# Optimization experiments

Hardware: AMD Instinct MI355X
Metric: run time of the kernel (lower is better)

The kernel has to match this reference:

```python
import jax, jax.numpy as jnp
import numpy as np

D_MODEL = 1024
HEAD_DIM = 64
NUM_HEADS = 16
NUM_KV_HEADS = 4
LOGIT_CAP = 50.0
F_EMBED = 10000


def rope(inputs, positions, head_dim, max_wavelength):
    # inputs: [B, T, N, H]; positions: [B, T]
    fraction = 2.0 * jnp.arange(head_dim // 2, dtype=jnp.float32) / head_dim
    timescale = max_wavelength ** fraction  # [H/2]
    sinusoid = positions.astype(jnp.float32)[..., None] / timescale  # [B, T, H/2]
    sinusoid = sinusoid[..., None, :]  # [B, T, 1, H/2]
    sin, cos = jnp.sin(sinusoid), jnp.cos(sinusoid)
    first, second = jnp.split(inputs, 2, axis=-1)
    return jnp.concatenate([first * cos - second * sin,
                            second * cos + first * sin], axis=-1)


def setup_inputs() -> dict:
    key = jax.random.key(0)
    kx, kq, kkv, ko = jax.random.split(key, 4)
    B, T = 1, 2048
    x = jax.random.normal(kx, (B, T, D_MODEL), dtype=jnp.float32)
    pos = jnp.broadcast_to(jnp.arange(T, dtype=jnp.int32)[None, :], (B, T))
    # mask semantics: True == masked out (logit set to -100). Causal: disallow s > t.
    mask = jnp.broadcast_to(jnp.triu(jnp.ones((T, T), dtype=bool), k=1)[None], (B, T, T))
    sq = 1.0 / np.sqrt(D_MODEL)
    wq = jax.random.normal(kq, (NUM_HEADS, D_MODEL, HEAD_DIM), dtype=jnp.float32) * sq
    wkv = jax.random.normal(kkv, (2, NUM_KV_HEADS, D_MODEL, HEAD_DIM), dtype=jnp.float32) * sq
    wout = jax.random.normal(ko, (NUM_HEADS, HEAD_DIM, D_MODEL), dtype=jnp.float32) * sq
    return {"x": x, "pos": pos, "mask": mask, "wq": wq, "wkv": wkv, "wout": wout}


def reference(x, pos, mask, wq, wkv, wout):
    B, T, _ = x.shape
    K, G = NUM_KV_HEADS, NUM_HEADS // NUM_KV_HEADS
    # projections
    q = jnp.einsum('BTD,NDH->BTNH', x, wq)  # [B,T,N,H]
    q = rope(q, pos, HEAD_DIM, F_EMBED) / jnp.sqrt(jnp.float32(HEAD_DIM))
    kv = jnp.einsum('BSD,CKDH->CBSKH', x, wkv)  # [2,B,S,K,H]
    k_proj, v_proj = kv[0], kv[1]
    k_proj = rope(k_proj, pos, HEAD_DIM, F_EMBED)
    # grouped logits
    qg = q.reshape(B, T, K, G, HEAD_DIM)
    logits = jnp.einsum('BTKGH,BSKH->BTKGS', qg, k_proj).reshape(B, T, NUM_HEADS, T)
    # soft-cap + mask (True in mask => masked => -100)
    logits = jnp.tanh(logits / LOGIT_CAP) * LOGIT_CAP
    logits = jnp.where(~mask[:, :, None, :], logits, -100.0)
    probs = jax.nn.softmax(logits, axis=-1).astype(k_proj.dtype)
    # grouped outer
    pg = probs.reshape(B, T, K, G, T)
    enc = jnp.einsum('BTKGS,BSKH->BTKGH', pg, v_proj).reshape(B, T, NUM_HEADS, HEAD_DIM)
    return jnp.einsum('BTNH,NHD->BTD', enc, wout)
```

## Files before the change

### kernel.cpp

```cpp
#include <hip/hip_runtime.h>
#include <hip/hip_bf16.h>
#include <cstdint>

#define T_SEQ 2048
#define DM    1024
#define HD    64
#define NH    16
#define NKV   4

typedef __attribute__((ext_vector_type(8))) short short8;
typedef __attribute__((ext_vector_type(4))) short short4v;
typedef __attribute__((ext_vector_type(2))) short short2v;
typedef __attribute__((ext_vector_type(4))) float f32x4;

__device__ __forceinline__ unsigned short f2bf(float f) {
    union { float f; unsigned u; } v; v.f = f;
    unsigned r = v.u + 0x7FFF + ((v.u >> 16) & 1);
    return (unsigned short)(r >> 16);
}

__device__ __forceinline__ void gload16(const unsigned short* gp, unsigned short* lp) {
    __builtin_amdgcn_global_load_lds(
        (const __attribute__((address_space(1))) unsigned int*)gp,
        (__attribute__((address_space(3))) unsigned int*)lp, 16, 0, 0);
}

__global__ __launch_bounds__(256) void prep_kernel(const float* __restrict__ x,
                                                   const int* __restrict__ pos,
                                                   const float* __restrict__ wq,
                                                   const float* __restrict__ wkv,
                                                   const float* __restrict__ wout,
                                                   unsigned short* __restrict__ xb,
                                                   float2* __restrict__ stab,
                                                   unsigned short* __restrict__ wqkvT,
                                                   unsigned short* __restrict__ woutT) {
    __shared__ unsigned short tile[64][65];
    int bid = blockIdx.x;
    if (bid < 1024) {
        int i = bid * 256 + threadIdx.x;
        const f32x4* xv = (const f32x4*)x + i * 2;
        f32x4 v0 = xv[0], v1 = xv[1];
        short8 o;
        #pragma unroll
        for (int j = 0; j < 4; j++) { o[j] = (short)f2bf(v0[j]); o[4 + j] = (short)f2bf(v1[j]); }
        *(short8*)(xb + i * 8) = o;
        if (i < 65536) {
            int tt = i >> 5, hm = i & 31;
            float ang = (float)pos[tt] * exp2f((float)hm * -0.41524101186092029f);
            float sv, cv;
            sincosf(ang, &sv, &cv);
            stab[i] = make_float2(sv, cv);
        }
    } else {
        int bid2 = bid - 1024;
        int d0 = (bid2 & 15) * 64;
        int bz = bid2 >> 4;
        int tc = threadIdx.x & 63, tr = threadIdx.x >> 6;
        int tc2 = threadIdx.x & 31, tr2 = threadIdx.x >> 5;
        if (bz < 24) {
            const float* src = (bz < 16) ? (wq + bz * 65536) : (wkv + (bz - 16) * 65536);
            #pragma unroll
            for (int rr = 0; rr < 64; rr += 4)
                tile[rr + tr][tc] = f2bf(src[(d0 + rr + tr) * 64 + tc]);
            __syncthreads();
            #pragma unroll
            for (int rr = 0; rr < 64; rr += 8) {
                int row = rr + tr2;
                short2v o2 = { (short)tile[2 * tc2][row], (short)tile[2 * tc2 + 1][row] };
                *(short2v*)&wqkvT[(bz * 64 + row) * 1024 + d0 + 2 * tc2] = o2;
            }
        } else {
            int j0 = (bz - 24) * 64;
            #pragma unroll
            for (int rr = 0; rr < 64; rr += 4)
                tile[rr + tr][tc] = f2bf(wout[(j0 + rr + tr) * 1024 + d0 + tc]);
            __syncthreads();
            #pragma unroll
            for (int rr = 0; rr < 64; rr += 8) {
                int row = rr + tr2;
                short2v o2 = { (short)tile[2 * tc2][row], (short)tile[2 * tc2 + 1][row] };
                *(short2v*)&woutT[(d0 + row) * 1024 + j0 + 2 * tc2] = o2;
            }
        }
    }
}

__global__ __launch_bounds__(256) void gemm_qkv(const unsigned short* __restrict__ A,
                                                const unsigned short* __restrict__ Bt,
                                                const float2* __restrict__ stab,
                                                unsigned short* __restrict__ qb,
                                                unsigned short* __restrict__ kb2,
                                                unsigned short* __restrict__ vT) {
    __shared__ unsigned short lA[2][4096];
    __shared__ unsigned short lB[2][4096];
    __shared__ float etile[64][65];

    int wid = threadIdx.x >> 6;
    int lane = threadIdx.x & 63;
    int l15 = lane & 15, g = lane >> 4;
    int wr = wid >> 1, wc = wid & 1;
    int r0 = blockIdx.x * 64;
    int by = blockIdx.y;
    int c0 = by * 64;

    f32x4 acc[2][2];
    #pragma unroll
    for (int m = 0; m < 2; m++)
        #pragma unroll
        for (int n = 0; n < 2; n++)
            acc[m][n] = (f32x4){0.f, 0.f, 0.f, 0.f};

    auto stage = [&](int buf, int k0) {
        #pragma unroll
        for (int chunk = 0; chunk < 2; chunk++) {
            int off = threadIdx.x * 16;
            int row = off >> 6, koff = (off & 63) >> 1;
            gload16(A + (r0 + row) * DM + k0 + chunk * 32 + koff,
                    &lA[buf][chunk * 2048 + (off >> 1)]);
            gload16(Bt + (c0 + row) * DM + k0 + chunk * 32 + koff,
                    &lB[buf][chunk * 2048 + (off >> 1)]);
        }
    };

    stage(0, 0);
    __syncthreads();
    for (int k0 = 0; k0 < DM; k0 += 64) {
        int buf = (k0 >> 6) & 1;
        if (k0 + 64 < DM) stage(buf ^ 1, k0 + 64);
        #pragma unroll
        for (int chunk = 0; chunk < 2; chunk++) {
            short8 af[2], bfr[2];
            #pragma unroll
            for (int m = 0; m < 2; m++)
                af[m] = *(const short8*)&lA[buf][chunk * 2048 + (wr * 32 + m * 16 + l15) * 32 + g * 8];
            #pragma unroll
            for (int n = 0; n < 2; n++)
                bfr[n] = *(const short8*)&lB[buf][chunk * 2048 + (wc * 32 + n * 16 + l15) * 32 + g * 8];
            __builtin_amdgcn_s_setprio(1);
            #pragma unroll
            for (int m = 0; m < 2; m++)
                #pragma unroll
                for (int n = 0; n < 2; n++)
                    acc[m][n] = __builtin_amdgcn_mfma_f32_16x16x32_bf16(af[m], bfr[n], acc[m][n], 0, 0, 0);
            __builtin_amdgcn_s_setprio(0);
        }
        __syncthreads();
    }

    #pragma unroll
    for (int m = 0; m < 2; m++)
        #pragma unroll
        for (int n = 0; n < 2; n++)
            #pragma unroll
            for (int rr = 0; rr < 4; rr++)
                etile[wr * 32 + m * 16 + g * 4 + rr][wc * 32 + n * 16 + l15] = acc[m][n][rr];
    __syncthreads();

    if (by < 20) {
        int row = threadIdx.x >> 2;
        int h0 = (threadIdx.x & 3) * 16;
        int t = r0 + row;
        float res[16];
        #pragma unroll
        for (int j = 0; j < 16; j++) {
            int h = h0 + j;
            float val = etile[row][h];
            float oth = etile[row][h ^ 32];
            float2 sc = stab[t * 32 + (h & 31)];
            res[j] = (h < 32) ? (val * sc.y - oth * sc.x) : (val * sc.y + oth * sc.x);
        }
        if (by < 16) {
            short8 o[2];
            #pragma unroll
            for (int j = 0; j < 16; j++) o[j >> 3][j & 7] = (short)f2bf(res[j] * 0.125f);
            unsigned short* qrow = qb + t * 1024 + by * 64 + h0;
            *(short8*)qrow = o[0];
            *(short8*)(qrow + 8) = o[1];
        } else {
            int kvh = by - 16;
            int swz = (t & 7) << 3;
            short8 o[2];
            #pragma unroll
            for (int j = 0; j < 16; j++) o[j >> 3][j & 7] = (short)f2bf(res[j]);
            unsigned short* krow = kb2 + kvh * (T_SEQ * 64) + t * 64;
            *(short8*)(krow + (h0 ^ swz)) = o[0];
            *(short8*)(krow + ((h0 + 8) ^ swz)) = o[1];
        }
    } else {
        int cgl = threadIdx.x >> 2;
        int u0 = (threadIdx.x & 3) * 16;
        int cglob = (by - 20) * 64 + cgl;
        int cx = cgl & 7;
        short8 o[2];
        #pragma unroll
        for (int j = 0; j < 16; j++) {
            int u = u0 + j;
            int chunk = u >> 3, qin = u & 7;
            int hi = qin >> 2, r = qin & 3;
            int sg = chunk ^ cx;
            int tl = (sg >> 2) * 32 + hi * 16 + (sg & 3) * 4 + r;
            o[j >> 3][j & 7] = (short)f2bf(etile[tl][cgl]);
        }
        unsigned short* vrow = vT + cglob * 2048 + r0 + u0;
        *(short8*)vrow = o[0];
        *(short8*)(vrow + 8) = o[1];
    }
}

template<int BM, int BN, int BK>
__global__ __launch_bounds__(256) void gemm_lds(const unsigned short* __restrict__ A,
                                                const unsigned short* __restrict__ Bt,
                                                float* __restrict__ C,
                                                int K, int lda, int ldb, int ldc) {
    constexpr int MR = BM / 32;
    constexpr int NC = BN / 32;
    constexpr int NCH = BK / 32;
    __shared__ unsigned short lA[2][BM * BK];
    __shared__ unsigned short lB[2][BN * BK];

    int wid = threadIdx.x >> 6;
    int lane = threadIdx.x & 63;
    int l15 = lane & 15, g = lane >> 4;
    int wr = wid >> 1, wc = wid & 1;
    int r0 = blockIdx.x * BM;
    int c0 = blockIdx.y * BN;

    f32x4 acc[MR][NC];
    #pragma unroll
    for (int m = 0; m < MR; m++)
        #pragma unroll
        for (int n = 0; n < NC; n++)
            acc[m][n] = (f32x4){0.f, 0.f, 0.f, 0.f};

    auto stage = [&](int buf, int k0) {
        #pragma unroll
        for (int chunk = 0; chunk < NCH; chunk++) {
            #pragma unroll
            for (int i = 0; i < BM / 64; i++) {
                int off = i * 4096 + threadIdx.x * 16;
                int row = off >> 6, koff = (off & 63) >> 1;
                gload16(A + (r0 + row) * lda + k0 + chunk * 32 + koff,
                        &lA[buf][chunk * BM * 32 + (off >> 1)]);
            }
            #pragma unroll
            for (int i = 0; i < BN / 64; i++) {
                int off = i * 4096 + threadIdx.x * 16;
                int row = off >> 6, koff = (off & 63) >> 1;
                gload16(Bt + (c0 + row) * ldb + k0 + chunk * 32 + koff,
                        &lB[buf][chunk * BN * 32 + (off >> 1)]);
            }
        }
    };

    stage(0, 0);
    __syncthreads();
    for (int k0 = 0; k0 < K; k0 += BK) {
        int buf = (k0 / BK) & 1;
        if (k0 + BK < K) stage(buf ^ 1, k0 + BK);
        #pragma unroll
        for (int chunk = 0; chunk < NCH; chunk++) {
            short8 af[MR], bfr[NC];
            #pragma unroll
            for (int m = 0; m < MR; m++)
                af[m] = *(const short8*)&lA[buf][chunk * BM * 32 + (wr * (BM / 2) + m * 16 + l15) * 32 + g * 8];
            #pragma unroll
            for (int n = 0; n < NC; n++)
                bfr[n] = *(const short8*)&lB[buf][chunk * BN * 32 + (wc * (BN / 2) + n * 16 + l15) * 32 + g * 8];
            __builtin_amdgcn_s_setprio(1);
            #pragma unroll
            for (int m = 0; m < MR; m++)
                #pragma unroll
                for (int n = 0; n < NC; n++)
                    acc[m][n] = __builtin_amdgcn_mfma_f32_16x16x32_bf16(af[m], bfr[n], acc[m][n], 0, 0, 0);
            __builtin_amdgcn_s_setprio(0);
        }
        __syncthreads();
    }
    #pragma unroll
    for (int m = 0; m < MR; m++) {
        int row = r0 + wr * (BM / 2) + m * 16 + g * 4;
        #pragma unroll
        for (int n = 0; n < NC; n++) {
            int col = c0 + wc * (BN / 2) + n * 16 + l15;
            #pragma unroll
            for (int rr = 0; rr < 4; rr++)
                C[(row + rr) * ldc + col] = acc[m][n][rr];
        }
    }
}

__global__ __launch_bounds__(512, 4) void attn_kernel(const unsigned short* __restrict__ qb,
                                                      const unsigned short* __restrict__ kb2,
                                                      const unsigned short* __restrict__ vT,
                                                      unsigned short* __restrict__ enc) {
    __shared__ unsigned short lk[2][8192];
    __shared__ unsigned short lv[2][8192];
    __shared__ float s_lc[3][4][16];

    int u = blockIdx.x;
    int kvh = u & 3;
    int j = u >> 2;
    int qt = (j < 64) ? j : (191 - j);
    int wid = threadIdx.x >> 6;
    int lane = threadIdx.x & 63;
    int l15 = lane & 15, g = lane >> 4;
    int hp = wid >> 2;
    int c = wid & 3;
    int q0 = qt * 16;
    int t = q0 + l15;
    int head0 = kvh * 4 + hp * 2;

    short8 qf0[2], qf1[2];
    #pragma unroll
    for (int e = 0; e < 2; e++) {
        const unsigned short* qrow = qb + t * 1024 + (head0 + e) * 64;
        qf0[e] = *(const short8*)(qrow + g * 8);
        qf1[e] = *(const short8*)(qrow + 32 + g * 8);
    }

    f32x4 acc[2][4];
    #pragma unroll
    for (int e = 0; e < 2; e++)
        #pragma unroll
        for (int ht = 0; ht < 4; ht++)
            acc[e][ht] = (f32x4){0.f, 0.f, 0.f, 0.f};
    float lrun[2] = {0.f, 0.f};
    int nph = qt / 8 + 1;

    auto stage = [&](int buf, int s0) {
        #pragma unroll
        for (int i = 0; i < 4; i++) {
            if (wid < 4) {
                int seg = wid * 4 + i;
                gload16(kb2 + kvh * (T_SEQ * 64) + s0 * 64 + seg * 512 + lane * 8,
                        &lk[buf][seg * 512]);
            } else {
                int sv = (wid - 4) * 4 + i;
                int h = sv * 4 + (lane >> 4);
                gload16(vT + (kvh * 64 + h) * T_SEQ + s0 + (lane & 15) * 8,
                        &lv[buf][sv * 512]);
            }
        }
    };

    stage(0, 0);
    __syncthreads();

    for (int ph = 0; ph < nph; ph++) {
        int buf = ph & 1;
        if (ph + 1 < nph) stage(buf ^ 1, (ph + 1) * 128);
        int s0c = ph * 128 + c * 32;
        if (s0c <= q0 + 15) {
            bool needmask = (s0c + 31 > q0);
            union PU { short8 s8; unsigned w[4]; } pf[2];
            #pragma unroll
            for (int uu = 0; uu < 2; uu++) {
                int srow = c * 32 + uu * 16 + l15;
                int swz = (srow & 7) << 3;
                short8 kf0 = *(const short8*)(&lk[buf][srow * 64 + ((g * 8) ^ swz)]);
                short8 kf1 = *(const short8*)(&lk[buf][srow * 64 + ((32 + g * 8) ^ swz)]);
                #pragma unroll
                for (int e = 0; e < 2; e++) {
                    f32x4 z = {0.f, 0.f, 0.f, 0.f};
                    __builtin_amdgcn_s_setprio(1);
                    z = __builtin_amdgcn_mfma_f32_16x16x32_bf16(kf0, qf0[e], z, 0, 0, 0);
                    z = __builtin_amdgcn_mfma_f32_16x16x32_bf16(kf1, qf1[e], z, 0, 0, 0);
                    __builtin_amdgcn_s_setprio(0);
                    float pv[4];
                    #pragma unroll
                    for (int r = 0; r < 4; r++) {
                        float x = z[r];
                        float xc = fmaf(x * x, x * (-1.3333333e-4f), x);
                        float pe = __builtin_amdgcn_exp2f(xc * 1.44269504f);
                        if (needmask) {
                            int s = s0c + uu * 16 + 4 * g + r;
                            pe = (s <= t) ? pe : 0.f;
                        }
                        lrun[e] += pe;
                        pv[r] = pe;
                    }
                    unsigned pk0, pk1;
                    asm("v_cvt_pk_bf16_f32 %0, %1, %2" : "=v"(pk0) : "v"(pv[0]), "v"(pv[1]));
                    asm("v_cvt_pk_bf16_f32 %0, %1, %2" : "=v"(pk1) : "v"(pv[2]), "v"(pv[3]));
                    pf[e].w[uu * 2] = pk0;
                    pf[e].w[uu * 2 + 1] = pk1;
                }
            }
            __builtin_amdgcn_s_setprio(1);
            #pragma unroll
            for (int ht = 0; ht < 4; ht++) {
                int h = ht * 16 + l15;
                short8 vf = *(const short8*)(&lv[buf][h * 128 + (c >> 1) * 64 +
                                                      (((c & 1) * 32 + g * 8) ^ ((h & 7) << 3))]);
                #pragma unroll
                for (int e = 0; e < 2; e++)
                    acc[e][ht] = __builtin_amdgcn_mfma_f32_16x16x32_bf16(vf, pf[e].s8, acc[e][ht], 0, 0, 0);
            }
            __builtin_amdgcn_s_setprio(0);
        }
        __syncthreads();
    }

    #pragma unroll
    for (int e = 0; e < 2; e++) {
        lrun[e] += __shfl_xor(lrun[e], 16);
        lrun[e] += __shfl_xor(lrun[e], 32);
    }

    float* L0 = (float*)&lk[0][0];
    float* L1 = L0 + 4096;
    float* L2 = (float*)&lv[0][0];
    if (c > 0) {
        float* layer = (c == 1) ? L0 : (c == 2) ? L1 : L2;
        #pragma unroll
        for (int e = 0; e < 2; e++) {
            if (g == 0) s_lc[c - 1][hp * 2 + e][l15] = lrun[e];
            #pragma unroll
            for (int ht = 0; ht < 4; ht++) {
                int idx = ((hp * 2 + e) * 16 + l15) * 64 + ((ht * 16 + 4 * g) ^ ((l15 & 3) << 3));
                *(f32x4*)&layer[idx] = acc[e][ht];
            }
        }
    }
    __syncthreads();
    if (c == 0) {
        #pragma unroll
        for (int e = 0; e < 2; e++) {
            float L = lrun[e] + s_lc[0][hp * 2 + e][l15] + s_lc[1][hp * 2 + e][l15]
                    + s_lc[2][hp * 2 + e][l15];
            float inv = 1.f / L;
            unsigned short* erow = enc + t * 1024 + (head0 + e) * 64;
            #pragma unroll
            for (int ht = 0; ht < 4; ht++) {
                int idx = ((hp * 2 + e) * 16 + l15) * 64 + ((ht * 16 + 4 * g) ^ ((l15 & 3) << 3));
                f32x4 sum = acc[e][ht] + *(const f32x4*)&L0[idx]
                          + *(const f32x4*)&L1[idx] + *(const f32x4*)&L2[idx];
                short4v o;
                #pragma unroll
                for (int r = 0; r < 4; r++)
                    o[r] = (short)f2bf(sum[r] * inv);
                *(short4v*)(erow + ht * 16 + 4 * g) = o;
            }
        }
    }
}

extern "C" void kernel_launch(void* const* d_in, const int* in_sizes, int n_in,
                              void* d_out, int out_size, void* d_ws, size_t ws_size,
                              hipStream_t stream) {
    (void)in_sizes; (void)n_in; (void)out_size; (void)ws_size;
    const float* x    = (const float*)d_in[0];
    const int*   pos  = (const int*)d_in[1];
    const float* wq   = (const float*)d_in[3];
    const float* wkv  = (const float*)d_in[4];
    const float* wout = (const float*)d_in[5];
    float* out = (float*)d_out;

    unsigned short* xb    = (unsigned short*)d_ws;
    unsigned short* wqkvT = xb + T_SEQ * DM;
    unsigned short* woutT = wqkvT + 1536 * DM;
    unsigned short* qb    = woutT + DM * DM;
    unsigned short* kb2   = qb + T_SEQ * DM;
    unsigned short* vT    = kb2 + NKV * T_SEQ * 64;
    unsigned short* enc   = vT + 256 * T_SEQ;
    float2* stab          = (float2*)(enc + T_SEQ * DM);

    prep_kernel<<<1664, 256, 0, stream>>>(x, pos, wq, wkv, wout, xb, stab, wqkvT, woutT);
    gemm_qkv<<<dim3(32, 24), 256, 0, stream>>>(xb, wqkvT, stab, qb, kb2, vT);
    attn_kernel<<<512, 512, 0, stream>>>(qb, kb2, vT, enc);
    gemm_lds<64, 64, 128><<<dim3(32, 16), 256, 0, stream>>>(enc, woutT, out, DM, DM, DM, DM);
}
```

Measured before the change: 62.55 us.

## Triple-buffer GEMM K-loops with single barrier and explicit vmcnt waits

Both the QKV projection GEMM and the output-projection GEMM move from a double-buffered K-loop with two syncs per step to a three-stage LDS ring. Loads run two tiles ahead, and each step uses one `s_waitcnt vmcnt(4)` plus one barrier. The output GEMM's K step drops from 128 to 64 so three buffers fit in LDS. In the QKV kernel, the epilogue tile now aliases the same shared buffer to keep LDS at 48KB. The aim is to hide global-load latency and cut barrier stalls. The cost is more LDS per block, which could lower occupancy, and a hand-tuned wait count that depends on how many loads each stage issues.

```diff
diff --git a/kernel.cpp b/kernel.cpp
--- a/kernel.cpp
+++ b/kernel.cpp
@@ -91,9 +91,10 @@
                                                 unsigned short* __restrict__ qb,
                                                 unsigned short* __restrict__ kb2,
                                                 unsigned short* __restrict__ vT) {
-    __shared__ unsigned short lA[2][4096];
-    __shared__ unsigned short lB[2][4096];
-    __shared__ float etile[64][65];
+    __shared__ __align__(16) unsigned char smem[49152];
+    unsigned short (*lA)[4096] = (unsigned short (*)[4096])smem;
+    unsigned short (*lB)[4096] = (unsigned short (*)[4096])(smem + 24576);
+    float (*etile)[65] = (float (*)[65])smem;
 
     int wid = threadIdx.x >> 6;
     int lane = threadIdx.x & 63;
@@ -121,12 +122,7 @@
                     &lB[buf][chunk * 2048 + (off >> 1)]);
         }
     };
-
-    stage(0, 0);
-    __syncthreads();
-    for (int k0 = 0; k0 < DM; k0 += 64) {
-        int buf = (k0 >> 6) & 1;
-        if (k0 + 64 < DM) stage(buf ^ 1, k0 + 64);
+    auto compute = [&](int buf) {
         #pragma unroll
         for (int chunk = 0; chunk < 2; chunk++) {
             short8 af[2], bfr[2];
@@ -144,8 +140,23 @@
                     acc[m][n] = __builtin_amdgcn_mfma_f32_16x16x32_bf16(af[m], bfr[n], acc[m][n], 0, 0, 0);
             __builtin_amdgcn_s_setprio(0);
         }
-        __syncthreads();
-    }
+    };
+
+    stage(0, 0);
+    stage(1, 64);
+    #pragma unroll 1
+    for (int i = 0; i < 15; i++) {
+        asm volatile("s_waitcnt vmcnt(4)" ::: "memory");
+        __builtin_amdgcn_s_barrier();
+        __builtin_amdgcn_sched_barrier(0);
+        if (i + 2 < 16) stage((i + 2) % 3, (i + 2) * 64);
+        compute(i % 3);
+    }
+    asm volatile("s_waitcnt vmcnt(0)" ::: "memory");
+    __builtin_amdgcn_s_barrier();
+    __builtin_amdgcn_sched_barrier(0);
+    compute(0);
+    __syncthreads();
 
     #pragma unroll
     for (int m = 0; m < 2; m++)
@@ -207,16 +218,15 @@
     }
 }
 
-template<int BM, int BN, int BK>
+template<int BM, int BN>
 __global__ __launch_bounds__(256) void gemm_lds(const unsigned short* __restrict__ A,
                                                 const unsigned short* __restrict__ Bt,
                                                 float* __restrict__ C,
                                                 int K, int lda, int ldb, int ldc) {
     constexpr int MR = BM / 32;
     constexpr int NC = BN / 32;
-    constexpr int NCH = BK / 32;
-    __shared__ unsigned short lA[2][BM * BK];
-    __shared__ unsigned short lB[2][BN * BK];
+    __shared__ unsigned short lA[3][BM * 64];
+    __shared__ unsigned short lB[3][BN * 64];
 
     int wid = threadIdx.x >> 6;
     int lane = threadIdx.x & 63;
@@ -234,7 +244,7 @@
 
     auto stage = [&](int buf, int k0) {
         #pragma unroll
-        for (int chunk = 0; chunk < NCH; chunk++) {
+        for (int chunk = 0; chunk < 2; chunk++) {
             #pragma unroll
             for (int i = 0; i < BM / 64; i++) {
                 int off = i * 4096 + threadIdx.x * 16;
@@ -251,14 +261,9 @@
             }
         }
     };
-
-    stage(0, 0);
-    __syncthreads();
-    for (int k0 = 0; k0 < K; k0 += BK) {
-        int buf = (k0 / BK) & 1;
-        if (k0 + BK < K) stage(buf ^ 1, k0 + BK);
-        #pragma unroll
-        for (int chunk = 0; chunk < NCH; chunk++) {
+    auto compute = [&](int buf) {
+        #pragma unroll
+        for (int chunk = 0; chunk < 2; chunk++) {
             short8 af[MR], bfr[NC];
             #pragma unroll
             for (int m = 0; m < MR; m++)
@@ -274,8 +279,24 @@
                     acc[m][n] = __builtin_amdgcn_mfma_f32_16x16x32_bf16(af[m], bfr[n], acc[m][n], 0, 0, 0);
             __builtin_amdgcn_s_setprio(0);
         }
-        __syncthreads();
-    }
+    };
+
+    int nIt = K >> 6;
+    stage(0, 0);
+    stage(1, 64);
+    #pragma unroll 1
+    for (int i = 0; i < nIt - 1; i++) {
+        asm volatile("s_waitcnt vmcnt(4)" ::: "memory");
+        __builtin_amdgcn_s_barrier();
+        __builtin_amdgcn_sched_barrier(0);
+        if (i + 2 < nIt) stage((i + 2) % 3, (i + 2) * 64);
+        compute(i % 3);
+    }
+    asm volatile("s_waitcnt vmcnt(0)" ::: "memory");
+    __builtin_amdgcn_s_barrier();
+    __builtin_amdgcn_sched_barrier(0);
+    compute((nIt - 1) % 3);
+
     #pragma unroll
     for (int m = 0; m < MR; m++) {
         int row = r0 + wr * (BM / 2) + m * 16 + g * 4;
@@ -468,5 +489,5 @@
     prep_kernel<<<1664, 256, 0, stream>>>(x, pos, wq, wkv, wout, xb, stab, wqkvT, woutT);
     gemm_qkv<<<dim3(32, 24), 256, 0, stream>>>(xb, wqkvT, stab, qb, kb2, vT);
     attn_kernel<<<512, 512, 0, stream>>>(qb, kb2, vT, enc);
-    gemm_lds<64, 64, 128><<<dim3(32, 16), 256, 0, stream>>>(enc, woutT, out, DM, DM, DM, DM);
-}
+    gemm_lds<64, 64><<<dim3(32, 16), 256, 0, stream>>>(enc, woutT, out, DM, DM, DM, DM);
+}
```

Measured after the change: 64.24 us. 2.7% more time.
